# Kernel tuning notes

Hardware: AMD Instinct MI355X
Metric: run time of the kernel (lower is better)

Reference implementation:

```python
import jax, jax.numpy as jnp
import numpy as np

N = 1_000_000
C = 128
NBINS = 15


def setup_inputs() -> dict:
    key = jax.random.key(0)
    k1, k2 = jax.random.split(key)
    logits = jax.random.normal(k1, (N, C), dtype=jnp.float32)
    labels = jax.random.randint(k2, (N,), 0, C, dtype=jnp.int64)
    return {"logits": logits, "labels": labels}


def reference(logits, labels):
    n = logits.shape[0]
    probs = jax.nn.softmax(logits, axis=1)
    confidences = jnp.max(probs, axis=1)                      # [N]
    predictions = jnp.argmax(probs, axis=1)                   # [N]
    accuracies = (predictions == labels).astype(jnp.float32)  # [N]

    # Equal-count (adaptive) bin edges: interp(linspace(0,N,nbins+1), arange(N), sort(conf))
    sorted_conf = jnp.sort(confidences)
    q = jnp.linspace(0.0, float(n), NBINS + 1)
    edges = jnp.interp(q, jnp.arange(n, dtype=jnp.float32), sorted_conf)  # [NBINS+1]

    # Bin i covers (edges[i], edges[i+1]] to match conf.gt(lower) & conf.le(upper).
    idx = jnp.searchsorted(edges[1:-1], confidences, side="left")  # [N] in [0, NBINS-1]
    valid = (confidences > edges[0]) & (confidences <= edges[-1])
    idx = jnp.where(valid, idx, NBINS)  # dump out-of-range into extra segment

    cnt = jax.ops.segment_sum(jnp.ones_like(confidences), idx, num_segments=NBINS + 1)[:NBINS]
    csum = jax.ops.segment_sum(confidences, idx, num_segments=NBINS + 1)[:NBINS]
    asum = jax.ops.segment_sum(accuracies, idx, num_segments=NBINS + 1)[:NBINS]

    prop = cnt / jnp.float32(n)
    safe = jnp.maximum(cnt, 1.0)
    gap = jnp.abs(csum / safe - asum / safe)
    ece = jnp.sum(jnp.where(cnt > 0, gap * prop, 0.0))
    return ece.reshape(1)
```

## Files before the change

kernel.cpp:

```cpp
#include <hip/hip_runtime.h>
#include <hip/hip_bf16.h>
#include <cstdint>

#define NROWS 1000000
#define NCLS  128
#define NBINS 15

#define FBASE 0x3B000000u
#define NB    73728
#define SCAN_T 1024
#define PER   (NB / SCAN_T)

#define OFF_CONF   0u
#define OFF_ACC    4000000u
#define OFF_HIST   5000000u
#define OFF_SUB    5294912u
#define OFF_PART   5417792u
#define OFF_TGTB   5466944u
#define OFF_TGTL   5467064u
#define OFF_EDGES  5467184u
#define ZERO_BYTES (OFF_PART - OFF_HIST)

#define DPP_FMAX(v, CTRL) { int _t = __builtin_amdgcn_update_dpp(                 \
        __float_as_int(v), __float_as_int(v), CTRL, 0xF, 0xF, false);             \
        (v) = fmaxf((v), __int_as_float(_t)); }
#define DPP_FADD(v, CTRL) { int _t = __builtin_amdgcn_update_dpp(                 \
        0, __float_as_int(v), CTRL, 0xF, 0xF, true);                              \
        (v) = (v) + __int_as_float(_t); }
#define CTRL_SHR1 0x111
#define CTRL_SHR2 0x112
#define CTRL_SHR4 0x114
#define CTRL_SHR8 0x118

__global__ __launch_bounds__(256) void k_row(const float* __restrict__ logits,
                                             const int* __restrict__ labels,
                                             float* __restrict__ conf,
                                             unsigned char* __restrict__ acc,
                                             unsigned int* __restrict__ hist)
{
    const int lane = threadIdx.x & 63;
    const int wv   = threadIdx.x >> 6;
    const int g    = lane >> 4;
    const int l16  = lane & 15;
    const int wbase = blockIdx.x * 32 + wv * 8;
    const float4* lg4 = reinterpret_cast<const float4*>(logits);

#pragma unroll
    for (int half = 0; half < 2; half++) {
        const int row = wbase + half * 4 + g;
        const float4 v0 = lg4[row * 32 + l16];
        const float4 v1 = lg4[row * 32 + 16 + l16];
        const int lab = labels[row];

        float m = fmaxf(fmaxf(fmaxf(v0.x, v0.y), fmaxf(v0.z, v0.w)),
                        fmaxf(fmaxf(v1.x, v1.y), fmaxf(v1.z, v1.w)));
        DPP_FMAX(m, CTRL_SHR1); DPP_FMAX(m, CTRL_SHR2);
        DPP_FMAX(m, CTRL_SHR4); DPP_FMAX(m, CTRL_SHR8);

        float s = __expf(v0.x) + __expf(v0.y) + __expf(v0.z) + __expf(v0.w)
                + __expf(v1.x) + __expf(v1.y) + __expf(v1.z) + __expf(v1.w);
        DPP_FADD(s, CTRL_SHR1); DPP_FADD(s, CTRL_SHR2);
        DPP_FADD(s, CTRL_SHR4); DPP_FADD(s, CTRL_SHR8);

        const bool hiHalf = (lab & 64) != 0;
        const float cx = hiHalf ? v1.x : v0.x;
        const float cy = hiHalf ? v1.y : v0.y;
        const float cz = hiHalf ? v1.z : v0.z;
        const float cw = hiHalf ? v1.w : v0.w;
        const int e = lab & 3;
        const float cand = (e == 0) ? cx : (e == 1) ? cy : (e == 2) ? cz : cw;
        float lv = (((lab >> 2) & 15) == l16) ? cand : __int_as_float(0xFF800000);
        DPP_FMAX(lv, CTRL_SHR1); DPP_FMAX(lv, CTRL_SHR2);
        DPP_FMAX(lv, CTRL_SHR4); DPP_FMAX(lv, CTRL_SHR8);

        if (l16 == 15) {
            const float c = __expf(m) / s;
            conf[row] = c;
            acc[row]  = (lv == m) ? 1u : 0u;
            int ub = (int)(__float_as_uint(c) - FBASE);
            int b  = ub >> 10;
            b = b < 0 ? 0 : (b >= NB ? NB - 1 : b);
            atomicAdd(&hist[b], 1u);
        }
    }
}

__device__ __forceinline__ unsigned int rank_of(int s)
{
    if (s == 0)  return 0u;
    if (s == 29) return (unsigned int)(NROWS - 1);
    int i = (s + 1) >> 1;
    unsigned int k = (unsigned int)((long long)i * NROWS / 15);
    return k + ((s & 1) ? 0u : 1u);
}

__global__ __launch_bounds__(SCAN_T) void k_scan(const unsigned int* __restrict__ hist,
                                                 int* __restrict__ tgtb,
                                                 int* __restrict__ tgtl)
{
    __shared__ unsigned int wtot[16], wpre[16];
    const int t = threadIdx.x;
    const int w = t >> 6, lane = t & 63;

    const uint4* h4 = reinterpret_cast<const uint4*>(hist + t * PER);
    unsigned int s = 0;
#pragma unroll
    for (int j = 0; j < PER / 4; j++) { uint4 u = h4[j]; s += u.x + u.y + u.z + u.w; }

    unsigned int incl = s;
#pragma unroll
    for (int off = 1; off < 64; off <<= 1) {
        unsigned int x = __shfl_up(incl, off);
        if (lane >= off) incl += x;
    }
    if (lane == 63) wtot[w] = incl;
    __syncthreads();
    if (t == 0) {
        unsigned int run = 0;
        for (int i = 0; i < 16; i++) { wpre[i] = run; run += wtot[i]; }
    }
    __syncthreads();
    const unsigned int run0 = wpre[w] + incl - s;

    for (int s2 = 0; s2 < 30; s2++) {
        unsigned int r = rank_of(s2);
        if (r >= run0 && r < run0 + s) {
            unsigned int run = run0;
            for (int j = 0; j < PER; j++) {
                unsigned int c = hist[t * PER + j];
                if (r < run + c) { tgtb[s2] = t * PER + j; tgtl[s2] = (int)(r - run); break; }
                run += c;
            }
        }
    }
}

__global__ __launch_bounds__(256) void k_subhist(const float* __restrict__ conf,
                                                 const int* __restrict__ tgtb,
                                                 unsigned int* __restrict__ sub)
{
    __shared__ int tb[32];
    if (threadIdx.x < 32) tb[threadIdx.x] = (threadIdx.x < 30) ? tgtb[threadIdx.x] : 0x7FFFFFFF;
    __syncthreads();
    const int stride = gridDim.x * blockDim.x;
    for (int i = blockIdx.x * blockDim.x + threadIdx.x; i < NROWS / 4; i += stride) {
        float4 c4 = reinterpret_cast<const float4*>(conf)[i];
        float cv[4] = {c4.x, c4.y, c4.z, c4.w};
#pragma unroll
        for (int e = 0; e < 4; e++) {
            int ub = (int)(__float_as_uint(cv[e]) - FBASE);
            int b  = ub >> 10;
            b = b < 0 ? 0 : (b >= NB ? NB - 1 : b);
            int lo10 = ub & 1023;
            int lo = (tb[15] < b) ? 16 : 0;
            lo += (tb[lo + 7] < b) ? 8 : 0;
            lo += (tb[lo + 3] < b) ? 4 : 0;
            lo += (tb[lo + 1] < b) ? 2 : 0;
            lo += (tb[lo]     < b) ? 1 : 0;
            if (tb[lo] == b) atomicAdd(&sub[lo * 1024 + lo10], 1u);
        }
    }
}

__global__ __launch_bounds__(1024) void k_edges(const unsigned int* __restrict__ sub,
                        const int* __restrict__ tgtb,
                        const int* __restrict__ tgtl,
                        float* __restrict__ edges)
{
    __shared__ float val[32];
    __shared__ int tb[30], rep[30];
    if (threadIdx.x < 30) tb[threadIdx.x] = tgtb[threadIdx.x];
    __syncthreads();
    if (threadIdx.x < 30) {
        int r = 0;
        while (tb[r] != tb[threadIdx.x]) r++;
        rep[threadIdx.x] = r;
    }
    __syncthreads();
    const int g = threadIdx.x >> 5;
    const int k = threadIdx.x & 31;
    if (g < 30) {
        const unsigned int local = (unsigned int)tgtl[g];
        unsigned int cs[32];
        unsigned int csum = 0;
        const unsigned int* p = sub + rep[g] * 1024 + k * 32;
#pragma unroll
        for (int j = 0; j < 32; j++) { cs[j] = p[j]; csum += cs[j]; }
        unsigned int incl = csum;
#pragma unroll
        for (int off = 1; off < 32; off <<= 1) {
            unsigned int x = __shfl_up(incl, off);
            if (k >= off) incl += x;
        }
        const unsigned int excl = incl - csum;
        if (local >= excl && local < excl + csum) {
            unsigned int run = excl;
            int subidx = 0;
#pragma unroll
            for (int j = 0; j < 32; j++) {
                if (local >= run && local < run + cs[j]) subidx = k * 32 + j;
                run += cs[j];
            }
            unsigned int bits = FBASE + ((unsigned int)tb[g] << 10) + (unsigned int)subidx;
            val[g] = __uint_as_float(bits);
        }
    }
    __syncthreads();
    if (threadIdx.x == 0) {
        edges[0]  = val[0];
        edges[15] = val[29];
        for (int i = 1; i <= 14; i++) {
            double q = (double)i * (double)NROWS / 15.0;
            long long kk = (long long)i * NROWS / 15;
            double f = q - (double)kk;
            edges[i] = (float)((1.0 - f) * (double)val[2 * i - 1] + f * (double)val[2 * i]);
        }
    }
}

__global__ __launch_bounds__(256) void k_bin(const float* __restrict__ conf,
                                             const unsigned char* __restrict__ acc,
                                             const float* __restrict__ edges,
                                             float* __restrict__ partial)
{
    __shared__ float se[16];
    __shared__ float sl[3][64 * 17];
    if (threadIdx.x < 16) se[threadIdx.x] = edges[threadIdx.x];
    for (int i = threadIdx.x; i < 3 * 64 * 17; i += 256) (&sl[0][0])[i] = 0.f;
    __syncthreads();

    const int slice = threadIdx.x & 63;
    const int stride = gridDim.x * blockDim.x;
    for (int i = blockIdx.x * blockDim.x + threadIdx.x; i < NROWS / 4; i += stride) {
        float4 c4 = reinterpret_cast<const float4*>(conf)[i];
        uchar4 a4 = reinterpret_cast<const uchar4*>(acc)[i];
        float cv[4] = {c4.x, c4.y, c4.z, c4.w};
        unsigned char av[4] = {a4.x, a4.y, a4.z, a4.w};
#pragma unroll
        for (int e = 0; e < 4; e++) {
            float v = cv[e];
            if (v > se[0] && v <= se[15]) {
                int idx = 0;
#pragma unroll
                for (int j = 1; j <= 14; j++) idx += (se[j] < v) ? 1 : 0;
                atomicAdd(&sl[0][slice * 17 + idx], 1.0f);
                atomicAdd(&sl[1][slice * 17 + idx], v);
                atomicAdd(&sl[2][slice * 17 + idx], (float)av[e]);
            }
        }
    }
    __syncthreads();
    if (threadIdx.x < 48) {
        const int a = threadIdx.x >> 4, b = threadIdx.x & 15;
        float sum = 0.f;
        for (int s = 0; s < 64; s++) sum += sl[a][s * 17 + b];
        partial[(a * 16 + b) * 256 + blockIdx.x] = sum;
    }
}

__global__ __launch_bounds__(1024) void k_final(const float* __restrict__ partial,
                                                float* __restrict__ out)
{
    __shared__ double tot[48];
    const int w    = threadIdx.x >> 6;
    const int lane = threadIdx.x & 63;
    for (int j = w; j < 48; j += 16) {
        double s = 0.0;
#pragma unroll
        for (int i = 0; i < 4; i++) s += (double)partial[j * 256 + i * 64 + lane];
#pragma unroll
        for (int d = 1; d < 64; d <<= 1) s += __shfl_xor(s, d);
        if (lane == 0) tot[j] = s;
    }
    __syncthreads();
    if (threadIdx.x == 0) {
        double ece = 0.0;
        for (int b = 0; b < NBINS; b++) {
            double cnt = tot[b];
            if (cnt > 0.0) {
                double safe = cnt < 1.0 ? 1.0 : cnt;
                double gap  = fabs(tot[16 + b] / safe - tot[32 + b] / safe);
                ece += gap * (cnt / (double)NROWS);
            }
        }
        out[0] = (float)ece;
    }
}

extern "C" void kernel_launch(void* const* d_in, const int* in_sizes, int n_in,
                              void* d_out, int out_size, void* d_ws, size_t ws_size,
                              hipStream_t stream)
{
    const float* logits = (const float*)d_in[0];
    const int*   labels = (const int*)d_in[1];
    char* ws = (char*)d_ws;

    float*         conf  = (float*)(ws + OFF_CONF);
    unsigned char* acc   = (unsigned char*)(ws + OFF_ACC);
    unsigned int*  hist  = (unsigned int*)(ws + OFF_HIST);
    unsigned int*  sub   = (unsigned int*)(ws + OFF_SUB);
    float*         part  = (float*)(ws + OFF_PART);
    int*           tgtb  = (int*)(ws + OFF_TGTB);
    int*           tgtl  = (int*)(ws + OFF_TGTL);
    float*         edges = (float*)(ws + OFF_EDGES);

    hipMemsetAsync(ws + OFF_HIST, 0, ZERO_BYTES, stream);

    k_row<<<NROWS / 32, 256, 0, stream>>>(logits, labels, conf, acc, hist);
    k_scan<<<1, SCAN_T, 0, stream>>>(hist, tgtb, tgtl);
    k_subhist<<<1024, 256, 0, stream>>>(conf, tgtb, sub);
    k_edges<<<1, 1024, 0, stream>>>(sub, tgtb, tgtl, edges);
    k_bin<<<256, 256, 0, stream>>>(conf, acc, edges, part);
    k_final<<<1, 1024, 0, stream>>>(part, (float*)d_out);
}
```

Measured before the change: 210.0 us.

## Process one softmax row per thread instead of sixteen lanes per row

The row kernel now assigns a whole 128-logit row to each thread, reading 32 float4 values sequentially and reducing max and exp-sum in registers. It also reads the label's logit directly, replacing the cross-lane DPP reductions and label-selection shuffle. This removes the cross-lane reductions and lets every thread write its own result and do its own histogram atomic. The cost is uncoalesced loads: adjacent threads now read addresses 512 bytes apart, which can hurt memory efficiency on a bandwidth-bound 512 MB read. Register pressure also rises.

```diff
diff --git a/kernel.cpp b/kernel.cpp
--- a/kernel.cpp
+++ b/kernel.cpp
@@ -21,68 +21,49 @@
 #define OFF_EDGES  5467184u
 #define ZERO_BYTES (OFF_PART - OFF_HIST)
 
-#define DPP_FMAX(v, CTRL) { int _t = __builtin_amdgcn_update_dpp(                 \
-        __float_as_int(v), __float_as_int(v), CTRL, 0xF, 0xF, false);             \
-        (v) = fmaxf((v), __int_as_float(_t)); }
-#define DPP_FADD(v, CTRL) { int _t = __builtin_amdgcn_update_dpp(                 \
-        0, __float_as_int(v), CTRL, 0xF, 0xF, true);                              \
-        (v) = (v) + __int_as_float(_t); }
-#define CTRL_SHR1 0x111
-#define CTRL_SHR2 0x112
-#define CTRL_SHR4 0x114
-#define CTRL_SHR8 0x118
-
 __global__ __launch_bounds__(256) void k_row(const float* __restrict__ logits,
                                              const int* __restrict__ labels,
                                              float* __restrict__ conf,
                                              unsigned char* __restrict__ acc,
                                              unsigned int* __restrict__ hist)
 {
-    const int lane = threadIdx.x & 63;
-    const int wv   = threadIdx.x >> 6;
-    const int g    = lane >> 4;
-    const int l16  = lane & 15;
-    const int wbase = blockIdx.x * 32 + wv * 8;
-    const float4* lg4 = reinterpret_cast<const float4*>(logits);
-
-#pragma unroll
-    for (int half = 0; half < 2; half++) {
-        const int row = wbase + half * 4 + g;
-        const float4 v0 = lg4[row * 32 + l16];
-        const float4 v1 = lg4[row * 32 + 16 + l16];
-        const int lab = labels[row];
-
-        float m = fmaxf(fmaxf(fmaxf(v0.x, v0.y), fmaxf(v0.z, v0.w)),
-                        fmaxf(fmaxf(v1.x, v1.y), fmaxf(v1.z, v1.w)));
-        DPP_FMAX(m, CTRL_SHR1); DPP_FMAX(m, CTRL_SHR2);
-        DPP_FMAX(m, CTRL_SHR4); DPP_FMAX(m, CTRL_SHR8);
-
-        float s = __expf(v0.x) + __expf(v0.y) + __expf(v0.z) + __expf(v0.w)
-                + __expf(v1.x) + __expf(v1.y) + __expf(v1.z) + __expf(v1.w);
-        DPP_FADD(s, CTRL_SHR1); DPP_FADD(s, CTRL_SHR2);
-        DPP_FADD(s, CTRL_SHR4); DPP_FADD(s, CTRL_SHR8);
-
-        const bool hiHalf = (lab & 64) != 0;
-        const float cx = hiHalf ? v1.x : v0.x;
-        const float cy = hiHalf ? v1.y : v0.y;
-        const float cz = hiHalf ? v1.z : v0.z;
-        const float cw = hiHalf ? v1.w : v0.w;
-        const int e = lab & 3;
-        const float cand = (e == 0) ? cx : (e == 1) ? cy : (e == 2) ? cz : cw;
-        float lv = (((lab >> 2) & 15) == l16) ? cand : __int_as_float(0xFF800000);
-        DPP_FMAX(lv, CTRL_SHR1); DPP_FMAX(lv, CTRL_SHR2);
-        DPP_FMAX(lv, CTRL_SHR4); DPP_FMAX(lv, CTRL_SHR8);
-
-        if (l16 == 15) {
-            const float c = __expf(m) / s;
-            conf[row] = c;
-            acc[row]  = (lv == m) ? 1u : 0u;
-            int ub = (int)(__float_as_uint(c) - FBASE);
-            int b  = ub >> 10;
-            b = b < 0 ? 0 : (b >= NB ? NB - 1 : b);
-            atomicAdd(&hist[b], 1u);
-        }
-    }
+    const int row = blockIdx.x * 256 + threadIdx.x;
+    if (row >= NROWS) return;
+    const float4* p = reinterpret_cast<const float4*>(logits) + (long long)row * 32;
+
+    float m = -1e30f, s = 0.f;
+#pragma unroll
+    for (int o = 0; o < 4; o++) {
+        float4 a = p[o * 8 + 0], b = p[o * 8 + 1], c = p[o * 8 + 2], d = p[o * 8 + 3];
+        float4 e = p[o * 8 + 4], f = p[o * 8 + 5], g = p[o * 8 + 6], h = p[o * 8 + 7];
+        m = fmaxf(m, fmaxf(fmaxf(fmaxf(a.x, a.y), fmaxf(a.z, a.w)),
+                           fmaxf(fmaxf(b.x, b.y), fmaxf(b.z, b.w))));
+        m = fmaxf(m, fmaxf(fmaxf(fmaxf(c.x, c.y), fmaxf(c.z, c.w)),
+                           fmaxf(fmaxf(d.x, d.y), fmaxf(d.z, d.w))));
+        m = fmaxf(m, fmaxf(fmaxf(fmaxf(e.x, e.y), fmaxf(e.z, e.w)),
+                           fmaxf(fmaxf(f.x, f.y), fmaxf(f.z, f.w))));
+        m = fmaxf(m, fmaxf(fmaxf(fmaxf(g.x, g.y), fmaxf(g.z, g.w)),
+                           fmaxf(fmaxf(h.x, h.y), fmaxf(h.z, h.w))));
+        s += __expf(a.x) + __expf(a.y) + __expf(a.z) + __expf(a.w)
+           + __expf(b.x) + __expf(b.y) + __expf(b.z) + __expf(b.w)
+           + __expf(c.x) + __expf(c.y) + __expf(c.z) + __expf(c.w)
+           + __expf(d.x) + __expf(d.y) + __expf(d.z) + __expf(d.w)
+           + __expf(e.x) + __expf(e.y) + __expf(e.z) + __expf(e.w)
+           + __expf(f.x) + __expf(f.y) + __expf(f.z) + __expf(f.w)
+           + __expf(g.x) + __expf(g.y) + __expf(g.z) + __expf(g.w)
+           + __expf(h.x) + __expf(h.y) + __expf(h.z) + __expf(h.w);
+    }
+
+    const int lab = labels[row];
+    const float lv = logits[(long long)row * 128 + lab];
+    const float c = __expf(m) / s;
+
+    conf[row] = c;
+    acc[row]  = (lv == m) ? 1u : 0u;
+    int ub = (int)(__float_as_uint(c) - FBASE);
+    int b  = ub >> 10;
+    b = b < 0 ? 0 : (b >= NB ? NB - 1 : b);
+    atomicAdd(&hist[b], 1u);
 }
 
 __device__ __forceinline__ unsigned int rank_of(int s)
@@ -306,7 +287,7 @@
 
     hipMemsetAsync(ws + OFF_HIST, 0, ZERO_BYTES, stream);
 
-    k_row<<<NROWS / 32, 256, 0, stream>>>(logits, labels, conf, acc, hist);
+    k_row<<<(NROWS + 255) / 256, 256, 0, stream>>>(logits, labels, conf, acc, hist);
     k_scan<<<1, SCAN_T, 0, stream>>>(hist, tgtb, tgtl);
     k_subhist<<<1024, 256, 0, stream>>>(conf, tgtb, sub);
     k_edges<<<1, 1024, 0, stream>>>(sub, tgtb, tgtl, edges);
```

Result: slower. 266.6 us (+27.0%).
